# Optimization experiments

Measured on AMD Instinct MI355X. Metric: run time of the kernel, lower is better.

Reference implementation:

```python
import jax, jax.numpy as jnp
import numpy as np

B, S, D_MODEL, H = 4, 4096, 1024, 16
HD = D_MODEL // H  # head_dim = 64


def setup_inputs() -> dict:
    key = jax.random.key(0)
    kq, kk, kv, kw, kb = jax.random.split(key, 5)
    Q = jax.random.normal(kq, (B, S, D_MODEL), dtype=jnp.float32)
    K = jax.random.normal(kk, (B, S, D_MODEL), dtype=jnp.float32)
    V = jax.random.normal(kv, (B, S, D_MODEL), dtype=jnp.float32)
    # out_proj: nn.Linear(d_model, d_model)
    lim = 1.0 / np.sqrt(D_MODEL)
    W_out = jax.random.uniform(kw, (D_MODEL, D_MODEL), jnp.float32, -lim, lim)
    b_out = jax.random.uniform(kb, (D_MODEL,), jnp.float32, -lim, lim)
    return {"Q": Q, "K": K, "V": V, "W_out": W_out, "b_out": b_out}


def reference(Q, K, V, W_out, b_out):
    b, s, d = Q.shape
    # split heads: [B, H, S, HD]
    Qh = Q.reshape(b, s, H, HD).transpose(0, 2, 1, 3)
    Kh = K.reshape(b, s, H, HD).transpose(0, 2, 1, 3)
    Vh = V.reshape(b, s, H, HD).transpose(0, 2, 1, 3)
    # linear attention reorder: KV = K^T V -> [B, H, HD, HD]
    KV = jnp.einsum('bhsd,bhse->bhde', Kh, Vh)
    # z = Q @ KV -> [B, H, S, HD]
    z = jnp.einsum('bhsd,bhde->bhse', Qh, KV)
    # merge heads -> [B, S, D]
    z = z.transpose(0, 2, 1, 3).reshape(b, s, d)
    # out_proj (torch Linear: x @ W^T + b, here W_out stored [out,in])
    return z @ W_out.T + b_out
```

## Files before the change

### kernel.cpp

```cpp
#include <hip/hip_runtime.h>
#include <hip/hip_bf16.h>

#define B_ 4
#define S_ 4096
#define DM 1024
#define H_ 16
#define HD 64
#define BH (B_*H_)
#define SPLIT 8
#define CHUNK (S_/SPLIT)
#define SUB 64

typedef __attribute__((ext_vector_type(8))) __bf16 bf16x8;
typedef __attribute__((ext_vector_type(4))) __bf16 bf16x4;
typedef __attribute__((ext_vector_type(4))) float f32x4;

#define MFMA16(a,b,c) __builtin_amdgcn_mfma_f32_16x16x32_bf16((a),(b),(c),0,0,0)

__device__ __forceinline__ void gload_lds16(const void* g, void* l) {
  __builtin_amdgcn_global_load_lds(
      (const __attribute__((address_space(1))) void*)g,
      (__attribute__((address_space(3))) void*)l, 16, 0, 0);
}

__global__ __launch_bounds__(256)
void k0_convq(const float* __restrict__ Qg, __bf16* __restrict__ Qb) {
  const size_t t = (size_t)blockIdx.x * 256 + threadIdx.x;
#pragma unroll
  for (int it = 0; it < 4; ++it) {
    const size_t i = (size_t)it * 1048576 + t;
    f32x4 w = *reinterpret_cast<const f32x4*>(Qg + i * 4);
    bf16x4 o;
#pragma unroll
    for (int j = 0; j < 4; ++j) o[j] = (__bf16)w[j];
    *reinterpret_cast<bf16x4*>(Qb + i * 4) = o;
  }
}

__global__ __launch_bounds__(256)
void k1_kv(const float* __restrict__ Kg, const float* __restrict__ Vg,
           float* __restrict__ partial) {
  __shared__ __align__(16) float Kb[2][SUB][64];
  __shared__ __align__(16) float Vb[2][SUB][64];
  const int bid = blockIdx.x;
  const int split = bid >> 6, bh = bid & 63;
  const int b = bh >> 4, h = bh & 15;
  const int t = threadIdx.x, wid = t >> 6;
  const int s0 = split * CHUNK;
  const float* Ksrc = Kg + ((size_t)b * S_ + s0) * DM + h * HD;
  const float* Vsrc = Vg + ((size_t)b * S_ + s0) * DM + h * HD;
  const int d0 = (t >> 4) * 4, e0 = (t & 15) * 4;
  float acc[4][4] = {};

  auto stage = [&](int bi, int sc) {
    const char* Kp = (const char*)(Ksrc + (size_t)sc * SUB * DM);
    const char* Vp = (const char*)(Vsrc + (size_t)sc * SUB * DM);
#pragma unroll
    for (int it = 0; it < 4; ++it) {
      const int idx = it * 256 + t;
      const int row = idx >> 4, ch = idx & 15;
      const int ldso = (it * 256 + wid * 64) * 16;
      gload_lds16((const void*)(Kp + (size_t)row * (DM * 4) + ch * 16),
                  (void*)((char*)&Kb[bi][0][0] + ldso));
      gload_lds16((const void*)(Vp + (size_t)row * (DM * 4) + ch * 16),
                  (void*)((char*)&Vb[bi][0][0] + ldso));
    }
  };

  stage(0, 0);
  asm volatile("s_waitcnt vmcnt(0)" ::: "memory");
  __builtin_amdgcn_s_barrier();

  for (int hc = 0; hc < CHUNK / SUB; ++hc) {
    const int cur = hc & 1;
    if (hc + 1 < CHUNK / SUB) stage(cur ^ 1, hc + 1);
    const float* Ks = &Kb[cur][0][0];
    const float* Vs = &Vb[cur][0][0];
#pragma unroll 8
    for (int s = 0; s < SUB; ++s) {
      f32x4 kv = *reinterpret_cast<const f32x4*>(Ks + s * 64 + d0);
      f32x4 vv = *reinterpret_cast<const f32x4*>(Vs + s * 64 + e0);
#pragma unroll
      for (int i = 0; i < 4; ++i)
#pragma unroll
        for (int j = 0; j < 4; ++j)
          acc[i][j] = fmaf(kv[i], vv[j], acc[i][j]);
    }
    asm volatile("s_waitcnt vmcnt(0)" ::: "memory");
    __builtin_amdgcn_s_barrier();
  }

  float* dst = partial + ((size_t)(split * BH + bh) << 12);
#pragma unroll
  for (int i = 0; i < 4; ++i) {
    f32x4 o;
#pragma unroll
    for (int j = 0; j < 4; ++j) o[j] = acc[i][j];
    *reinterpret_cast<f32x4*>(dst + (d0 + i) * 64 + e0) = o;
  }
}

__global__ __launch_bounds__(256)
void k2_kv_reduce(const float* __restrict__ partial,
                  __bf16* __restrict__ kvt) {
  const int bid = blockIdx.x;
  const int bh = bid >> 2, q = bid & 3;
  const int t = threadIdx.x;
#pragma unroll
  for (int i = 0; i < 4; ++i) {
    const int idx = q * 1024 + i * 256 + t;
    float s = 0.f;
#pragma unroll
    for (int sp = 0; sp < SPLIT; ++sp)
      s += partial[((size_t)(sp * BH + bh) << 12) + idx];
    kvt[((size_t)bh << 12) + idx] = (__bf16)s;
  }
}

__global__ __launch_bounds__(256)
void k25_u(const float* __restrict__ Wg,
           const __bf16* __restrict__ kvt,
           __bf16* __restrict__ Ut) {
  const int bid = blockIdx.x;
  const int bh = bid >> 2, nblk = bid & 3;
  const int b = bh >> 4, h = bh & 15;
  const int t = threadIdx.x, w = t >> 6, l = t & 63, lr = l & 15, lg = l >> 4;
  const int n0w = nblk * 256 + w * 64;
  const __bf16* kvb = kvt + ((size_t)bh << 12);
  f32x4 acc[4][4] = {};
#pragma unroll
  for (int ks = 0; ks < 2; ++ks) {
    bf16x8 bfr[4];
#pragma unroll
    for (int nf = 0; nf < 4; ++nf)
      bfr[nf] = *reinterpret_cast<const bf16x8*>(kvb + (nf * 16 + lr) * 64 + ks * 32 + lg * 8);
#pragma unroll
    for (int mf = 0; mf < 4; ++mf) {
      const int n = n0w + mf * 16 + lr;
      const float* wp = Wg + (size_t)n * DM + h * 64 + ks * 32 + lg * 8;
      f32x4 w0 = *reinterpret_cast<const f32x4*>(wp);
      f32x4 w1 = *reinterpret_cast<const f32x4*>(wp + 4);
      bf16x8 af;
#pragma unroll
      for (int j = 0; j < 4; ++j) { af[j] = (__bf16)w0[j]; af[4 + j] = (__bf16)w1[j]; }
#pragma unroll
      for (int nf = 0; nf < 4; ++nf)
        acc[mf][nf] = MFMA16(af, bfr[nf], acc[mf][nf]);
    }
  }
  __bf16* ub = Ut + ((size_t)b << 20);
#pragma unroll
  for (int mf = 0; mf < 4; ++mf)
#pragma unroll
    for (int nf = 0; nf < 4; ++nf)
#pragma unroll
      for (int r = 0; r < 4; ++r) {
        const int n = n0w + mf * 16 + lg * 4 + r;
        ub[(size_t)n * DM + h * 64 + nf * 16 + lr] = (__bf16)acc[mf][nf][r];
      }
}

__global__ __launch_bounds__(256)
void k4_out_gemm(const __bf16* __restrict__ Qb,
                 const __bf16* __restrict__ Ut,
                 const float* __restrict__ biasg,
                 float* __restrict__ outg) {
  __shared__ __align__(16) __bf16 Alds[128 * 64];
  __shared__ __align__(16) __bf16 Blds[128 * 64];
  const int bid = blockIdx.x;
  const int b = bid >> 8, rem = bid & 255;
  const int nblk = rem >> 5, mblk = rem & 31;
  const int m0 = mblk * 128, n0 = nblk * 128;
  const int t = threadIdx.x, wid = t >> 6, l = t & 63, lr = l & 15, lg = l >> 4;
  const int wr = wid >> 1, wc = wid & 1;
  const __bf16* Ab = Qb + (size_t)b * S_ * DM;
  const __bf16* Bb = Ut + ((size_t)b << 20);
  f32x4 acc[4][4] = {};

  for (int kt = 0; kt < 16; ++kt) {
    const int k0 = kt * 64;
#pragma unroll
    for (int it = 0; it < 4; ++it) {
      const int idx = it * 256 + t;
      const int row = idx >> 3, c = idx & 7;
      const int gc = c ^ (row & 7);
      gload_lds16((const void*)(Ab + (size_t)(m0 + row) * DM + k0 + gc * 8),
                  (void*)((char*)Alds + (it * 256 + wid * 64) * 16));
      gload_lds16((const void*)(Bb + (size_t)(n0 + row) * DM + k0 + gc * 8),
                  (void*)((char*)Blds + (it * 256 + wid * 64) * 16));
    }
    __syncthreads();
#pragma unroll
    for (int ks = 0; ks < 2; ++ks) {
      bf16x8 af[4], bfr[4];
#pragma unroll
      for (int mt = 0; mt < 4; ++mt) {
        const int row = wr * 64 + mt * 16 + lr;
        const int ch = (ks * 4 + lg) ^ (row & 7);
        af[mt] = *reinterpret_cast<const bf16x8*>((const char*)Alds + row * 128 + ch * 16);
      }
#pragma unroll
      for (int nt = 0; nt < 4; ++nt) {
        const int row = wc * 64 + nt * 16 + lr;
        const int ch = (ks * 4 + lg) ^ (row & 7);
        bfr[nt] = *reinterpret_cast<const bf16x8*>((const char*)Blds + row * 128 + ch * 16);
      }
#pragma unroll
      for (int mt = 0; mt < 4; ++mt)
#pragma unroll
        for (int nt = 0; nt < 4; ++nt)
          acc[mt][nt] = MFMA16(af[mt], bfr[nt], acc[mt][nt]);
    }
    __syncthreads();
  }

#pragma unroll
  for (int nt = 0; nt < 4; ++nt) {
    const int colg = n0 + wc * 64 + nt * 16 + lr;
    const float bv = biasg[colg];
#pragma unroll
    for (int mt = 0; mt < 4; ++mt)
#pragma unroll
      for (int r = 0; r < 4; ++r) {
        const int rowg = m0 + wr * 64 + mt * 16 + lg * 4 + r;
        outg[((size_t)b * S_ + rowg) * DM + colg] = acc[mt][nt][r] + bv;
      }
  }
}

extern "C" void kernel_launch(void* const* d_in, const int* in_sizes, int n_in,
                              void* d_out, int out_size, void* d_ws, size_t ws_size,
                              hipStream_t stream) {
  const float* Q = (const float*)d_in[0];
  const float* K = (const float*)d_in[1];
  const float* V = (const float*)d_in[2];
  const float* W = (const float*)d_in[3];
  const float* bias = (const float*)d_in[4];
  float* out = (float*)d_out;

  char* ws = (char*)d_ws;
  float* partial = (float*)ws;
  __bf16* kvt = (__bf16*)(ws + (8u << 20));
  __bf16* Ut  = (__bf16*)(ws + (9u << 20));
  __bf16* Qb  = (__bf16*)(ws + (17u << 20));

  hipLaunchKernelGGL(k1_kv, dim3(SPLIT * BH), dim3(256), 0, stream, K, V, partial);
  hipLaunchKernelGGL(k0_convq, dim3(4096), dim3(256), 0, stream, Q, Qb);
  hipLaunchKernelGGL(k2_kv_reduce, dim3(BH * 4), dim3(256), 0, stream, partial, kvt);
  hipLaunchKernelGGL(k25_u, dim3(BH * 4), dim3(256), 0, stream, W, kvt, Ut);
  hipLaunchKernelGGL(k4_out_gemm, dim3(1024), dim3(256), 0, stream, Qb, Ut, bias, out);
}
```

Before: 124.6 us.

## Use 8x8 register tiles per thread in K^T V with intra-block wave split-S reduction

Each wave now covers every fourth row of the sequence chunk and computes the full 64x64 K^T V tile, with each thread holding an 8x8 accumulator instead of 4x4. The four per-wave partials are reduced through shared memory before the write. This doubles FMA work per LDS load to ease LDS bandwidth pressure in the outer-product loop. In exchange it raises register use (64 accumulators) and adds an LDS reduction pass at the end.

After: 128.1 us. 1.03x slower.

```diff
diff --git a/kernel.cpp b/kernel.cpp
--- a/kernel.cpp
+++ b/kernel.cpp
@@ -40,30 +40,29 @@
 __global__ __launch_bounds__(256)
 void k1_kv(const float* __restrict__ Kg, const float* __restrict__ Vg,
            float* __restrict__ partial) {
-  __shared__ __align__(16) float Kb[2][SUB][64];
-  __shared__ __align__(16) float Vb[2][SUB][64];
+  __shared__ __align__(16) float sh[16384];
   const int bid = blockIdx.x;
   const int split = bid >> 6, bh = bid & 63;
   const int b = bh >> 4, h = bh & 15;
-  const int t = threadIdx.x, wid = t >> 6;
+  const int t = threadIdx.x, w = t >> 6, l = t & 63;
   const int s0 = split * CHUNK;
   const float* Ksrc = Kg + ((size_t)b * S_ + s0) * DM + h * HD;
   const float* Vsrc = Vg + ((size_t)b * S_ + s0) * DM + h * HD;
-  const int d0 = (t >> 4) * 4, e0 = (t & 15) * 4;
-  float acc[4][4] = {};
+  const int td = (l >> 3) * 8, te = (l & 7) * 8;
+  float acc[8][8] = {};
 
   auto stage = [&](int bi, int sc) {
     const char* Kp = (const char*)(Ksrc + (size_t)sc * SUB * DM);
     const char* Vp = (const char*)(Vsrc + (size_t)sc * SUB * DM);
+    char* Kl = (char*)sh + bi * 16384;
+    char* Vl = (char*)sh + 32768 + bi * 16384;
 #pragma unroll
     for (int it = 0; it < 4; ++it) {
       const int idx = it * 256 + t;
       const int row = idx >> 4, ch = idx & 15;
-      const int ldso = (it * 256 + wid * 64) * 16;
-      gload_lds16((const void*)(Kp + (size_t)row * (DM * 4) + ch * 16),
-                  (void*)((char*)&Kb[bi][0][0] + ldso));
-      gload_lds16((const void*)(Vp + (size_t)row * (DM * 4) + ch * 16),
-                  (void*)((char*)&Vb[bi][0][0] + ldso));
+      const int ldso = (it * 256 + w * 64) * 16;
+      gload_lds16((const void*)(Kp + (size_t)row * 4096 + ch * 16), (void*)(Kl + ldso));
+      gload_lds16((const void*)(Vp + (size_t)row * 4096 + ch * 16), (void*)(Vl + ldso));
     }
   };
 
@@ -74,29 +73,52 @@
   for (int hc = 0; hc < CHUNK / SUB; ++hc) {
     const int cur = hc & 1;
     if (hc + 1 < CHUNK / SUB) stage(cur ^ 1, hc + 1);
-    const float* Ks = &Kb[cur][0][0];
-    const float* Vs = &Vb[cur][0][0];
-#pragma unroll 8
-    for (int s = 0; s < SUB; ++s) {
-      f32x4 kv = *reinterpret_cast<const f32x4*>(Ks + s * 64 + d0);
-      f32x4 vv = *reinterpret_cast<const f32x4*>(Vs + s * 64 + e0);
+    const float* Ks = sh + cur * 4096;
+    const float* Vs = sh + 8192 + cur * 4096;
+#pragma unroll 4
+    for (int si = 0; si < SUB / 4; ++si) {
+      const int s = si * 4 + w;
+      f32x4 ka = *reinterpret_cast<const f32x4*>(Ks + s * 64 + td);
+      f32x4 kb = *reinterpret_cast<const f32x4*>(Ks + s * 64 + td + 4);
+      f32x4 va = *reinterpret_cast<const f32x4*>(Vs + s * 64 + te);
+      f32x4 vb = *reinterpret_cast<const f32x4*>(Vs + s * 64 + te + 4);
 #pragma unroll
       for (int i = 0; i < 4; ++i)
 #pragma unroll
-        for (int j = 0; j < 4; ++j)
-          acc[i][j] = fmaf(kv[i], vv[j], acc[i][j]);
+        for (int j = 0; j < 4; ++j) {
+          acc[i][j]         = fmaf(ka[i], va[j], acc[i][j]);
+          acc[i][j + 4]     = fmaf(ka[i], vb[j], acc[i][j + 4]);
+          acc[i + 4][j]     = fmaf(kb[i], va[j], acc[i + 4][j]);
+          acc[i + 4][j + 4] = fmaf(kb[i], vb[j], acc[i + 4][j + 4]);
+        }
     }
     asm volatile("s_waitcnt vmcnt(0)" ::: "memory");
     __builtin_amdgcn_s_barrier();
   }
 
+  float* red = sh;
+#pragma unroll
+  for (int i = 0; i < 8; ++i)
+#pragma unroll
+    for (int jc = 0; jc < 2; ++jc) {
+      f32x4 o;
+#pragma unroll
+      for (int j = 0; j < 4; ++j) o[j] = acc[i][jc * 4 + j];
+      *reinterpret_cast<f32x4*>(red + w * 4096 + (td + i) * 64 + te + jc * 4) = o;
+    }
+  __builtin_amdgcn_s_barrier();
   float* dst = partial + ((size_t)(split * BH + bh) << 12);
 #pragma unroll
-  for (int i = 0; i < 4; ++i) {
+  for (int c2 = 0; c2 < 4; ++c2) {
+    const int base = (c2 * 256 + t) * 4;
+    f32x4 a0 = *reinterpret_cast<const f32x4*>(red + base);
+    f32x4 a1 = *reinterpret_cast<const f32x4*>(red + 4096 + base);
+    f32x4 a2 = *reinterpret_cast<const f32x4*>(red + 8192 + base);
+    f32x4 a3 = *reinterpret_cast<const f32x4*>(red + 12288 + base);
     f32x4 o;
 #pragma unroll
-    for (int j = 0; j < 4; ++j) o[j] = acc[i][j];
-    *reinterpret_cast<f32x4*>(dst + (d0 + i) * 64 + e0) = o;
+    for (int j = 0; j < 4; ++j) o[j] = (a0[j] + a1[j]) + (a2[j] + a3[j]);
+    *reinterpret_cast<f32x4*>(dst + base) = o;
   }
 }
 
```
